# Kernel optimization log

Measured on AMD Instinct MI355X. Metric: run time of the kernel, lower is better.

The kernel has to match this reference:

```python
import jax, jax.numpy as jnp
import numpy as np

H, W, NB, BS, D = 128, 256, 8, 96, 768
HIDDEN = 4 * D
LAMBDA = 0.01  # softshrink lambda (sparsity)
EPS = 1e-5     # torch LayerNorm default eps


def layernorm(x, g, b):
    mu = jnp.mean(x, axis=-1, keepdims=True)
    var = jnp.mean((x - mu) ** 2, axis=-1, keepdims=True)
    return (x - mu) * jax.lax.rsqrt(var + EPS) * g + b


def softshrink(x, lam):
    return jnp.sign(x) * jnp.maximum(jnp.abs(x) - lam, 0.0)


def afno(x, w1, w2, b1, b2):
    # x: [B, H*W, D]; bias branch is zeros since Block constructs AFNO with bias=None
    B, HW, Dd = x.shape
    xg = x.reshape(B, H, W, Dd)
    xf = jnp.fft.rfft2(xg, axes=(1, 2), norm='ortho')          # [B, H, W//2+1, D] complex
    xf = xf.reshape(B, H, W // 2 + 1, NB, BS)
    xr, xi = jnp.real(xf), jnp.imag(xf)

    def mul(t, w):  # block-diagonal channel mixing: [..., l, m] x [l, m, n]
        return jnp.einsum('bhwlm,lmn->bhwln', t, w)

    r1 = jax.nn.relu(mul(xr, w1[0]) - mul(xi, w1[1]) + b1[0])
    i1 = jax.nn.relu(mul(xr, w1[1]) + mul(xi, w1[0]) + b1[1])
    r2 = jax.nn.relu(mul(r1, w2[0]) - mul(i1, w2[1]) + b2[0])
    i2 = jax.nn.relu(mul(r1, w2[1]) + mul(i1, w2[0]) + b2[1])
    r2 = softshrink(r2, LAMBDA)
    i2 = softshrink(i2, LAMBDA)
    xc = (r2 + 1j * i2).reshape(B, H, W // 2 + 1, Dd)
    out = jnp.fft.irfft2(xc, s=(H, W), axes=(1, 2), norm='ortho')
    return out.reshape(B, HW, Dd)


def setup_inputs() -> dict:
    key = jax.random.key(0)
    ks = jax.random.split(key, 12)
    s = 0.02
    inp = {
        'x': jax.random.normal(ks[0], (2, H * W, D), dtype=jnp.float32),
        'norm1_g': jnp.ones((D,), jnp.float32),
        'norm1_b': jnp.zeros((D,), jnp.float32),
        'w1': s * jax.random.normal(ks[1], (2, NB, BS, BS), jnp.float32),
        'w2': s * jax.random.normal(ks[2], (2, NB, BS, BS), jnp.float32),
        'b1': s * jax.random.normal(ks[3], (2, NB, BS), jnp.float32),
        'b2': s * jax.random.normal(ks[4], (2, NB, BS), jnp.float32),
        'norm2_g': jnp.ones((D,), jnp.float32),
        'norm2_b': jnp.zeros((D,), jnp.float32),
        'fc1_w': s * jax.random.normal(ks[5], (D, HIDDEN), jnp.float32),
        'fc1_b': s * jax.random.normal(ks[6], (HIDDEN,), jnp.float32),
        'fc2_w': s * jax.random.normal(ks[7], (HIDDEN, D), jnp.float32),
        'fc2_b': s * jax.random.normal(ks[8], (D,), jnp.float32),
    }
    return inp


def reference(x, norm1_g, norm1_b, w1, w2, b1, b2, norm2_g, norm2_b,
              fc1_w, fc1_b, fc2_w, fc2_b):
    residual = x
    h = layernorm(x, norm1_g, norm1_b)
    h = afno(h, w1, w2, b1, b2)          # AFNO adds zero bias internally (bias=None)
    h = layernorm(h, norm2_g, norm2_b)
    h = jax.nn.gelu(h @ fc1_w + fc1_b, approximate=False)  # torch nn.GELU default = exact erf
    h = h @ fc2_w + fc2_b
    return h + residual
```

## Files before the change

kernel.cpp:

```cpp
#include <hip/hip_runtime.h>
#include <math.h>

#define Hh 128
#define Ww 256
#define Dd 768
#define NPLANE 256
#define WF 129
#define SFREQ (WF*Dd)
#define NPOS (2*Hh*WF)
#define LAMBDA_SS 0.01f

typedef short short8 __attribute__((ext_vector_type(8)));
typedef float floatx4 __attribute__((ext_vector_type(4)));

__device__ __forceinline__ float bf2f(ushort u) {
    union { unsigned int i; float f; } v; v.i = ((unsigned int)u) << 16; return v.f;
}
__device__ __forceinline__ ushort f2bf(float f) {
    union { float f; unsigned int i; } v; v.f = f;
    unsigned int r = v.i + 0x7fffu + ((v.i >> 16) & 1u);
    return (ushort)(r >> 16);
}

__global__ __launch_bounds__(256) void ln_kernel(const float* __restrict__ x,
        const float* __restrict__ g, const float* __restrict__ b,
        ushort* __restrict__ out) {
    int row = blockIdx.x;
    int tid = threadIdx.x;
    const float* xr = x + (size_t)row * Dd;
    float v0 = xr[tid], v1 = xr[tid + 256], v2 = xr[tid + 512];
    __shared__ float red[256];
    red[tid] = v0 + v1 + v2;
    __syncthreads();
    for (int o = 128; o > 0; o >>= 1) { if (tid < o) red[tid] += red[tid + o]; __syncthreads(); }
    float mean = red[0] * (1.0f / 768.0f);
    __syncthreads();
    float d0 = v0 - mean, d1 = v1 - mean, d2 = v2 - mean;
    red[tid] = d0 * d0 + d1 * d1 + d2 * d2;
    __syncthreads();
    for (int o = 128; o > 0; o >>= 1) { if (tid < o) red[tid] += red[tid + o]; __syncthreads(); }
    float inv = rsqrtf(red[0] * (1.0f / 768.0f) + 1e-5f);
    ushort* orow = out + (size_t)row * Dd;
    orow[tid]       = f2bf(d0 * inv * g[tid]       + b[tid]);
    orow[tid + 256] = f2bf(d1 * inv * g[tid + 256] + b[tid + 256]);
    orow[tid + 512] = f2bf(d2 * inv * g[tid + 512] + b[tid + 512]);
}

#define TW_WFC_H  0
#define TW_WFC_L  65536
#define TW_WFS_H  131072
#define TW_WFS_L  196608
#define TW_HC_H   262144
#define TW_HC_L   278528
#define TW_HS_H   294912
#define TW_HS_L   311296
#define TW_HSN_H  327680
#define TW_HSN_L  344064
#define TW_WIC_H  360448
#define TW_WIC_L  401408
#define TW_WISN_H 442368
#define TW_WISN_L 483328
#define TW_TOTAL  524288

__device__ __forceinline__ void split_bf(float v, ushort* hi, ushort* lo) {
    ushort h = f2bf(v);
    *hi = h;
    *lo = f2bf(v - bf2f(h));
}

__global__ __launch_bounds__(256) void twiddle_prep_kernel(ushort* __restrict__ tw) {
    int fam = blockIdx.y;
    int idx = blockIdx.x * 256 + threadIdx.x;
    if (fam == 0) {
        if (idx >= 65536) return;
        int wf = idx >> 8, w = idx & 255;
        float c = 0.0f, s = 0.0f;
        if (wf < WF) {
            int t = (w * wf) & 255;
            float ang = (float)t * (float)(2.0 * M_PI / 256.0);
            c = cosf(ang) * 0.0625f;
            s = -sinf(ang) * 0.0625f;
        }
        split_bf(c, &tw[TW_WFC_H + idx], &tw[TW_WFC_L + idx]);
        split_bf(s, &tw[TW_WFS_H + idx], &tw[TW_WFS_L + idx]);
    } else if (fam == 1) {
        if (idx >= 16384) return;
        int a = idx >> 7, b = idx & 127;
        int t = (a * b) & 127;
        float ang = (float)t * (float)(2.0 * M_PI / 128.0);
        const float sc = 0.08838834764831845f;
        float c = cosf(ang) * sc, s = sinf(ang) * sc;
        split_bf(c,  &tw[TW_HC_H + idx],  &tw[TW_HC_L + idx]);
        split_bf(s,  &tw[TW_HS_H + idx],  &tw[TW_HS_L + idx]);
        split_bf(-s, &tw[TW_HSN_H + idx], &tw[TW_HSN_L + idx]);
    } else {
        if (idx >= 40960) return;
        int w = idx / 160, wf = idx - w * 160;
        float c = 0.0f, s = 0.0f;
        if (wf < WF) {
            int t = (w * wf) & 255;
            float ang = (float)t * (float)(2.0 * M_PI / 256.0);
            float wt = (wf == 0 || wf == 128) ? 0.5f : 1.0f;
            c = wt * cosf(ang) * 0.125f;
            s = -wt * sinf(ang) * 0.125f;
        }
        split_bf(c, &tw[TW_WIC_H + idx],  &tw[TW_WIC_L + idx]);
        split_bf(s, &tw[TW_WISN_H + idx], &tw[TW_WISN_L + idx]);
    }
}

__global__ __launch_bounds__(256) void transpose_bf_kernel(const ushort* __restrict__ in,
        ushort* __restrict__ out, int R, int C, int Rpad, size_t inB, size_t outB) {
    __shared__ ushort tile[32][33];
    int z = blockIdx.z;
    int c0 = blockIdx.x * 32, r0 = blockIdx.y * 32;
    int tx = threadIdx.x, ty = threadIdx.y;
    const ushort* ip = in + (size_t)z * inB;
    ushort* op = out + (size_t)z * outB;
    for (int j = 0; j < 32; j += 8) {
        int r = r0 + ty + j;
        tile[ty + j][tx] = (r < R) ? ip[(size_t)r * C + c0 + tx] : (ushort)0;
    }
    __syncthreads();
    for (int j = 0; j < 32; j += 8)
        op[(size_t)(c0 + ty + j) * Rpad + r0 + tx] = tile[tx][ty + j];
}

__global__ __launch_bounds__(256) void dftg_kernel(
        const ushort* __restrict__ A1h, const ushort* __restrict__ A1l,
        const ushort* __restrict__ A2h, const ushort* __restrict__ A2l,
        const ushort* __restrict__ B1, const ushort* __restrict__ B2,
        void* __restrict__ Cv, int M, int N, int K,
        size_t strideB, size_t strideC, int out_f32) {
    __shared__ __align__(16) ushort Bs1[128 * 40];
    __shared__ __align__(16) ushort Bs2[128 * 40];
    int tid = threadIdx.x;
    int bn = blockIdx.x * 128, bm = blockIdx.y * 128;
    int z = blockIdx.z;
    const ushort* b1g = B1 + (size_t)z * strideB;
    const ushort* b2g = B2 + (size_t)z * strideB;
    int wave = tid >> 6, lane = tid & 63;
    int wy = wave >> 1, wx = wave & 1;
    int quad = lane >> 4, l16 = lane & 15;
    int sr = tid >> 2, sc = (tid & 3) * 8;
    int P2 = (A2h != nullptr);

    size_t arow = (size_t)(bm + wy * 64 + l16) * K + quad * 8;
    const ushort* a1h_p = A1h + arow;
    const ushort* a1l_p = A1l + arow;
    const ushort* a2h_p = (P2 ? A2h : A1h) + arow;
    const ushort* a2l_p = (P2 ? A2l : A1l) + arow;

    floatx4 acc[4][4];
#pragma unroll
    for (int i = 0; i < 4; ++i)
#pragma unroll
        for (int j = 0; j < 4; ++j) { acc[i][j][0] = 0.f; acc[i][j][1] = 0.f; acc[i][j][2] = 0.f; acc[i][j][3] = 0.f; }

    for (int k0 = 0; k0 < K; k0 += 32) {
        uint4 b1a = *(const uint4*)(b1g + (size_t)(bn + sr) * K + k0 + sc);
        uint4 b1b = *(const uint4*)(b1g + (size_t)(bn + sr + 64) * K + k0 + sc);
        uint4 b2a, b2b;
        if (P2) {
            b2a = *(const uint4*)(b2g + (size_t)(bn + sr) * K + k0 + sc);
            b2b = *(const uint4*)(b2g + (size_t)(bn + sr + 64) * K + k0 + sc);
        }
        __syncthreads();
        *(uint4*)&Bs1[sr * 40 + sc] = b1a;
        *(uint4*)&Bs1[(sr + 64) * 40 + sc] = b1b;
        if (P2) {
            *(uint4*)&Bs2[sr * 40 + sc] = b2a;
            *(uint4*)&Bs2[(sr + 64) * 40 + sc] = b2b;
        }
        __syncthreads();
        short8 bf1[4], bf2[4];
#pragma unroll
        for (int j = 0; j < 4; ++j)
            bf1[j] = *(const short8*)&Bs1[(wx * 64 + j * 16 + l16) * 40 + quad * 8];
        if (P2) {
#pragma unroll
            for (int j = 0; j < 4; ++j)
                bf2[j] = *(const short8*)&Bs2[(wx * 64 + j * 16 + l16) * 40 + quad * 8];
        }
#pragma unroll
        for (int i = 0; i < 4; ++i) {
            size_t ao = (size_t)i * 16 * K + k0;
            short8 a1h_ = *(const short8*)(a1h_p + ao);
            short8 a1l_ = *(const short8*)(a1l_p + ao);
#pragma unroll
            for (int j = 0; j < 4; ++j) {
                acc[i][j] = __builtin_amdgcn_mfma_f32_16x16x32_bf16(a1h_, bf1[j], acc[i][j], 0, 0, 0);
                acc[i][j] = __builtin_amdgcn_mfma_f32_16x16x32_bf16(a1l_, bf1[j], acc[i][j], 0, 0, 0);
            }
            if (P2) {
                short8 a2h_ = *(const short8*)(a2h_p + ao);
                short8 a2l_ = *(const short8*)(a2l_p + ao);
#pragma unroll
                for (int j = 0; j < 4; ++j) {
                    acc[i][j] = __builtin_amdgcn_mfma_f32_16x16x32_bf16(a2h_, bf2[j], acc[i][j], 0, 0, 0);
                    acc[i][j] = __builtin_amdgcn_mfma_f32_16x16x32_bf16(a2l_, bf2[j], acc[i][j], 0, 0, 0);
                }
            }
        }
    }

#pragma unroll
    for (int i = 0; i < 4; ++i) {
        int row0 = bm + wy * 64 + i * 16 + quad * 4;
#pragma unroll
        for (int j = 0; j < 4; ++j) {
            int col = bn + wx * 64 + j * 16 + l16;
#pragma unroll
            for (int r = 0; r < 4; ++r) {
                int row = row0 + r;
                if (row < M) {
                    size_t o = (size_t)z * strideC + (size_t)row * N + col;
                    if (out_f32) ((float*)Cv)[o] = acc[i][j][r];
                    else         ((ushort*)Cv)[o] = f2bf(acc[i][j][r]);
                }
            }
        }
    }
}

__global__ __launch_bounds__(256) void wmix_prep_kernel(const float* __restrict__ w,
        ushort* __restrict__ wt) {
    int mat = blockIdx.x;
    const float* src = w + (size_t)mat * 96 * 96;
    ushort* dst = wt + (size_t)mat * 96 * 96;
    for (int idx = threadIdx.x; idx < 96 * 96; idx += 256) {
        int n = idx / 96, m = idx - n * 96;
        dst[idx] = f2bf(src[(size_t)m * 96 + n]);
    }
}

__device__ __forceinline__ short8 neg8(short8 a) {
    union { short8 s; unsigned int u[4]; } v; v.s = a;
    v.u[0] ^= 0x80008000u; v.u[1] ^= 0x80008000u;
    v.u[2] ^= 0x80008000u; v.u[3] ^= 0x80008000u;
    return v.s;
}

#define WSTR 104
__global__ __launch_bounds__(256) void mix_mfma_kernel(const ushort* __restrict__ Xr,
        const ushort* __restrict__ Xi, const ushort* __restrict__ Wt,
        const float* __restrict__ bias, ushort* __restrict__ Or,
        ushort* __restrict__ Oi, int shrink) {
    int l = blockIdx.y;
    int bm = blockIdx.x * 128;
    int tid = threadIdx.x;
    int wv = tid >> 6, lane = tid & 63;
    int quad = lane >> 4, l16 = lane & 15;

    __shared__ __align__(16) ushort Wr_s[96 * WSTR];
    __shared__ __align__(16) ushort Wi_s[96 * WSTR];
    const ushort* wr_g = Wt + (size_t)l * 96 * 96;
    const ushort* wi_g = Wt + (size_t)(8 + l) * 96 * 96;
    for (int idx = tid; idx < (96 * 96) / 4; idx += 256) {
        int n = idx / 24, mq = idx - n * 24;
        *(uint2*)&Wr_s[n * WSTR + mq * 4] = *(const uint2*)(wr_g + (size_t)n * 96 + mq * 4);
        *(uint2*)&Wi_s[n * WSTR + mq * 4] = *(const uint2*)(wi_g + (size_t)n * 96 + mq * 4);
    }

    floatx4 accr[2][6], acci[2][6];
#pragma unroll
    for (int i = 0; i < 2; ++i)
#pragma unroll
        for (int j = 0; j < 6; ++j) {
            accr[i][j][0] = 0.f; accr[i][j][1] = 0.f; accr[i][j][2] = 0.f; accr[i][j][3] = 0.f;
            acci[i][j][0] = 0.f; acci[i][j][1] = 0.f; acci[i][j][2] = 0.f; acci[i][j][3] = 0.f;
        }

    int row = bm + wv * 32 + l16;
    const ushort* agr = Xr + (size_t)row * 768 + l * 96;
    const ushort* agi = Xi + (size_t)row * 768 + l * 96;
    __syncthreads();

#pragma unroll
    for (int ks = 0; ks < 3; ++ks) {
        int ko = ks * 32 + quad * 8;
        short8 ar0 = *(const short8*)(agr + ko);
        short8 ar1 = *(const short8*)(agr + (size_t)16 * 768 + ko);
        short8 ai0 = *(const short8*)(agi + ko);
        short8 ai1 = *(const short8*)(agi + (size_t)16 * 768 + ko);
        short8 an0 = neg8(ai0), an1 = neg8(ai1);
#pragma unroll
        for (int j = 0; j < 6; ++j) {
            short8 br = *(const short8*)&Wr_s[(j * 16 + l16) * WSTR + ko];
            short8 bi = *(const short8*)&Wi_s[(j * 16 + l16) * WSTR + ko];
            accr[0][j] = __builtin_amdgcn_mfma_f32_16x16x32_bf16(ar0, br, accr[0][j], 0, 0, 0);
            accr[0][j] = __builtin_amdgcn_mfma_f32_16x16x32_bf16(an0, bi, accr[0][j], 0, 0, 0);
            acci[0][j] = __builtin_amdgcn_mfma_f32_16x16x32_bf16(ar0, bi, acci[0][j], 0, 0, 0);
            acci[0][j] = __builtin_amdgcn_mfma_f32_16x16x32_bf16(ai0, br, acci[0][j], 0, 0, 0);
            accr[1][j] = __builtin_amdgcn_mfma_f32_16x16x32_bf16(ar1, br, accr[1][j], 0, 0, 0);
            accr[1][j] = __builtin_amdgcn_mfma_f32_16x16x32_bf16(an1, bi, accr[1][j], 0, 0, 0);
            acci[1][j] = __builtin_amdgcn_mfma_f32_16x16x32_bf16(ar1, bi, acci[1][j], 0, 0, 0);
            acci[1][j] = __builtin_amdgcn_mfma_f32_16x16x32_bf16(ai1, br, acci[1][j], 0, 0, 0);
        }
    }

#pragma unroll
    for (int i = 0; i < 2; ++i) {
        int row0 = bm + wv * 32 + i * 16 + quad * 4;
#pragma unroll
        for (int j = 0; j < 6; ++j) {
            int col = j * 16 + l16;
            float bvr = bias[l * 96 + col];
            float bvi = bias[768 + l * 96 + col];
#pragma unroll
            for (int r = 0; r < 4; ++r) {
                float vr = accr[i][j][r] + bvr;
                float vi = acci[i][j][r] + bvi;
                if (shrink) { vr = fmaxf(vr - LAMBDA_SS, 0.0f); vi = fmaxf(vi - LAMBDA_SS, 0.0f); }
                else        { vr = fmaxf(vr, 0.0f);             vi = fmaxf(vi, 0.0f); }
                size_t o = (size_t)(row0 + r) * 768 + l * 96 + col;
                Or[o] = f2bf(vr);
                Oi[o] = f2bf(vi);
            }
        }
    }
}

__global__ __launch_bounds__(256) void transpose_kernel(const float* __restrict__ in,
        ushort* __restrict__ out, int R, int C) {
    __shared__ float tile[32][33];
    int c0 = blockIdx.x * 32, r0 = blockIdx.y * 32;
    int tx = threadIdx.x, ty = threadIdx.y;
    for (int j = 0; j < 32; j += 8)
        tile[ty + j][tx] = in[(size_t)(r0 + ty + j) * C + c0 + tx];
    __syncthreads();
    for (int j = 0; j < 32; j += 8)
        out[(size_t)(c0 + ty + j) * R + r0 + tx] = f2bf(tile[tx][ty + j]);
}

#define GBM 128
#define GBN 128
#define GBK 32
__global__ __launch_bounds__(256) void gemm_bt_kernel(const ushort* __restrict__ A,
        const ushort* __restrict__ Bt, void* __restrict__ Cv, int M, int N, int K,
        const float* __restrict__ bias, const float* __restrict__ resid,
        int act, int out_f32) {
    __shared__ __align__(16) ushort As[GBM * GBK];
    __shared__ __align__(16) ushort Bs[GBN * GBK];
    int tid = threadIdx.x;
    int bm = blockIdx.y * GBM, bn = blockIdx.x * GBN;
    int wave = tid >> 6, lane = tid & 63;
    int wy = wave >> 1, wx = wave & 1;
    int quad = lane >> 4, l16 = lane & 15;
    int sr = tid >> 2;
    int sc = (tid & 3) * 8;
    const ushort* Ag = A + (size_t)(bm + sr) * K + sc;
    const ushort* Bg = Bt + (size_t)(bn + sr) * K + sc;

    floatx4 acc[4][4];
#pragma unroll
    for (int i = 0; i < 4; ++i)
#pragma unroll
        for (int j = 0; j < 4; ++j) { acc[i][j][0] = 0.f; acc[i][j][1] = 0.f; acc[i][j][2] = 0.f; acc[i][j][3] = 0.f; }

    for (int k0 = 0; k0 < K; k0 += GBK) {
        uint4 a0 = *(const uint4*)(Ag + k0);
        uint4 a1 = *(const uint4*)(Ag + (size_t)64 * K + k0);
        uint4 b0 = *(const uint4*)(Bg + k0);
        uint4 b1 = *(const uint4*)(Bg + (size_t)64 * K + k0);
        __syncthreads();
        *(uint4*)&As[sr * GBK + sc] = a0;
        *(uint4*)&As[(sr + 64) * GBK + sc] = a1;
        *(uint4*)&Bs[sr * GBK + sc] = b0;
        *(uint4*)&Bs[(sr + 64) * GBK + sc] = b1;
        __syncthreads();
        short8 af[4], bfv[4];
#pragma unroll
        for (int i = 0; i < 4; ++i)
            af[i] = *(const short8*)&As[(wy * 64 + i * 16 + l16) * GBK + quad * 8];
#pragma unroll
        for (int j = 0; j < 4; ++j)
            bfv[j] = *(const short8*)&Bs[(wx * 64 + j * 16 + l16) * GBK + quad * 8];
#pragma unroll
        for (int i = 0; i < 4; ++i)
#pragma unroll
            for (int j = 0; j < 4; ++j)
                acc[i][j] = __builtin_amdgcn_mfma_f32_16x16x32_bf16(af[i], bfv[j], acc[i][j], 0, 0, 0);
    }

#pragma unroll
    for (int i = 0; i < 4; ++i) {
        int row0 = bm + wy * 64 + i * 16 + quad * 4;
#pragma unroll
        for (int j = 0; j < 4; ++j) {
            int col = bn + wx * 64 + j * 16 + l16;
            float bv = bias ? bias[col] : 0.0f;
#pragma unroll
            for (int r = 0; r < 4; ++r) {
                float v = acc[i][j][r] + bv;
                if (act == 1) v = 0.5f * v * (1.0f + erff(v * 0.70710678118f));
                size_t o = (size_t)(row0 + r) * N + col;
                if (out_f32) {
                    float vv = v + (resid ? resid[o] : 0.0f);
                    ((float*)Cv)[o] = vv;
                } else {
                    ((ushort*)Cv)[o] = f2bf(v);
                }
            }
        }
    }
}

extern "C" void kernel_launch(void* const* d_in, const int* in_sizes, int n_in,
                              void* d_out, int out_size, void* d_ws, size_t ws_size,
                              hipStream_t stream) {
    const float* x    = (const float*)d_in[0];
    const float* n1g  = (const float*)d_in[1];
    const float* n1b  = (const float*)d_in[2];
    const float* w1   = (const float*)d_in[3];
    const float* w2   = (const float*)d_in[4];
    const float* b1   = (const float*)d_in[5];
    const float* b2   = (const float*)d_in[6];
    const float* n2g  = (const float*)d_in[7];
    const float* n2b  = (const float*)d_in[8];
    const float* fc1w = (const float*)d_in[9];
    const float* fc1b = (const float*)d_in[10];
    const float* fc2w = (const float*)d_in[11];
    const float* fc2b = (const float*)d_in[12];
    float*  outf = (float*)d_out;
    ushort* outu = (ushort*)d_out;

    ushort* ws  = (ushort*)d_ws;
    ushort* W1t = ws;
    ushort* W2t = W1t + (size_t)3072 * 768;
    ushort* tw  = W2t + (size_t)768 * 3072;
    ushort* AR  = tw + TW_TOTAL;

    const size_t FSZ = (size_t)NPLANE * SFREQ;
    ushort* S1t = AR;
    ushort* FrT = AR;
    ushort* FiT = AR + FSZ;
    ushort* Mr  = AR;
    ushort* Mi  = AR + FSZ;
    ushort* NrT = AR;
    ushort* NiT = AR + FSZ;
    ushort* HrT = AR;
    ushort* HiT = AR + (size_t)256 * 768 * 160;
    ushort* Abf = AR;
    ushort* hid = AR + (size_t)65536 * 768;

    ushort* S1 = outu;
    ushort* Fr = outu;
    ushort* Fi = outu + FSZ;
    ushort* Gr = outu;
    ushort* Gi = outu + FSZ;
    ushort* Nr = outu;
    ushort* Ni = outu + FSZ;
    ushort* Hr = outu;
    ushort* Hi = outu + FSZ;
    ushort* W1mix = outu + 2 * FSZ;
    ushort* W2mix = W1mix + (size_t)2 * 8 * 96 * 96;

    transpose_kernel<<<dim3(3072 / 32, 768 / 32), dim3(32, 8), 0, stream>>>(fc1w, W1t, 768, 3072);
    transpose_kernel<<<dim3(768 / 32, 3072 / 32), dim3(32, 8), 0, stream>>>(fc2w, W2t, 3072, 768);
    wmix_prep_kernel<<<16, 256, 0, stream>>>(w1, W1mix);
    wmix_prep_kernel<<<16, 256, 0, stream>>>(w2, W2mix);
    twiddle_prep_kernel<<<dim3(256, 3), 256, 0, stream>>>(tw);

    ln_kernel<<<65536, 256, 0, stream>>>(x, n1g, n1b, S1);

    transpose_bf_kernel<<<dim3(768 / 32, 256 / 32, 256), dim3(32, 8), 0, stream>>>(
        S1, S1t, 256, 768, 256, (size_t)256 * 768, (size_t)768 * 256);
    dftg_kernel<<<dim3(768 / 128, 2, 256), 256, 0, stream>>>(
        tw + TW_WFC_H, tw + TW_WFC_L, nullptr, nullptr, S1t, S1t,
        Fr, WF, 768, 256, (size_t)768 * 256, (size_t)SFREQ, 0);
    dftg_kernel<<<dim3(768 / 128, 2, 256), 256, 0, stream>>>(
        tw + TW_WFS_H, tw + TW_WFS_L, nullptr, nullptr, S1t, S1t,
        Fi, WF, 768, 256, (size_t)768 * 256, (size_t)SFREQ, 0);

    transpose_bf_kernel<<<dim3(SFREQ / 32, 128 / 32, 2), dim3(32, 8), 0, stream>>>(
        Fr, FrT, 128, SFREQ, 128, (size_t)128 * SFREQ, (size_t)128 * SFREQ);
    transpose_bf_kernel<<<dim3(SFREQ / 32, 128 / 32, 2), dim3(32, 8), 0, stream>>>(
        Fi, FiT, 128, SFREQ, 128, (size_t)128 * SFREQ, (size_t)128 * SFREQ);
    dftg_kernel<<<dim3(SFREQ / 128, 1, 2), 256, 0, stream>>>(
        tw + TW_HC_H, tw + TW_HC_L, tw + TW_HS_H, tw + TW_HS_L, FrT, FiT,
        Gr, 128, SFREQ, 128, (size_t)128 * SFREQ, (size_t)128 * SFREQ, 0);
    dftg_kernel<<<dim3(SFREQ / 128, 1, 2), 256, 0, stream>>>(
        tw + TW_HC_H, tw + TW_HC_L, tw + TW_HSN_H, tw + TW_HSN_L, FiT, FrT,
        Gi, 128, SFREQ, 128, (size_t)128 * SFREQ, (size_t)128 * SFREQ, 0);

    mix_mfma_kernel<<<dim3(NPOS / 128, 8), 256, 0, stream>>>(Gr, Gi, W1mix, b1, Mr, Mi, 0);
    mix_mfma_kernel<<<dim3(NPOS / 128, 8), 256, 0, stream>>>(Mr, Mi, W2mix, b2, Nr, Ni, 1);

    transpose_bf_kernel<<<dim3(SFREQ / 32, 128 / 32, 2), dim3(32, 8), 0, stream>>>(
        Nr, NrT, 128, SFREQ, 128, (size_t)128 * SFREQ, (size_t)128 * SFREQ);
    transpose_bf_kernel<<<dim3(SFREQ / 32, 128 / 32, 2), dim3(32, 8), 0, stream>>>(
        Ni, NiT, 128, SFREQ, 128, (size_t)128 * SFREQ, (size_t)128 * SFREQ);
    dftg_kernel<<<dim3(SFREQ / 128, 1, 2), 256, 0, stream>>>(
        tw + TW_HC_H, tw + TW_HC_L, tw + TW_HSN_H, tw + TW_HSN_L, NrT, NiT,
        Hr, 128, SFREQ, 128, (size_t)128 * SFREQ, (size_t)128 * SFREQ, 0);
    dftg_kernel<<<dim3(SFREQ / 128, 1, 2), 256, 0, stream>>>(
        tw + TW_HC_H, tw + TW_HC_L, tw + TW_HS_H, tw + TW_HS_L, NiT, NrT,
        Hi, 128, SFREQ, 128, (size_t)128 * SFREQ, (size_t)128 * SFREQ, 0);

    transpose_bf_kernel<<<dim3(768 / 32, 5, 256), dim3(32, 8), 0, stream>>>(
        Hr, HrT, WF, 768, 160, (size_t)SFREQ, (size_t)768 * 160);
    transpose_bf_kernel<<<dim3(768 / 32, 5, 256), dim3(32, 8), 0, stream>>>(
        Hi, HiT, WF, 768, 160, (size_t)SFREQ, (size_t)768 * 160);
    dftg_kernel<<<dim3(768 / 128, 2, 256), 256, 0, stream>>>(
        tw + TW_WIC_H, tw + TW_WIC_L, tw + TW_WISN_H, tw + TW_WISN_L, HrT, HiT,
        outf, 256, 768, 160, (size_t)768 * 160, (size_t)256 * 768, 1);

    ln_kernel<<<65536, 256, 0, stream>>>(outf, n2g, n2b, Abf);

    const int CH = 8192;
    for (int c = 0; c < 8; ++c) {
        const ushort* Aln = Abf + (size_t)c * CH * 768;
        gemm_bt_kernel<<<dim3(3072 / GBN, CH / GBM), 256, 0, stream>>>(
            Aln, W1t, hid, CH, 3072, 768, fc1b, nullptr, 1, 0);
        gemm_bt_kernel<<<dim3(768 / GBN, CH / GBM), 256, 0, stream>>>(
            hid, W2t, outf + (size_t)c * CH * 768, CH, 768, 3072, fc2b,
            x + (size_t)c * CH * 768, 0, 1);
    }
}
```

Before: 3.140 ms.

## Fuse real/imag DFT GEMM pairs into single kernels with LDS-staged coalesced stores

Pairs of DFT GEMM launches that read the same B operand (real and imaginary outputs) are merged into one dftc kernel. It computes both accumulators from one staged B tile, using sign-flipped A fragments for the complex cross terms. Outputs are staged through shared memory so the kernel can write coalesced 16-byte stores instead of scattered scalar stores, and the final inverse-W DFT gets its own specialised kernel with an fp32 staged epilogue. This halves the B-operand traffic and the launch count, but doubles accumulator registers, which may cut occupancy despite the launch_bounds(256,2) hint.

Measured after the change: 2.991 ms. 4.7% less time.

```diff
diff --git a/kernel.cpp b/kernel.cpp
--- a/kernel.cpp
+++ b/kernel.cpp
@@ -20,6 +20,12 @@
     union { float f; unsigned int i; } v; v.f = f;
     unsigned int r = v.i + 0x7fffu + ((v.i >> 16) & 1u);
     return (ushort)(r >> 16);
+}
+__device__ __forceinline__ short8 neg8(short8 a) {
+    union { short8 s; unsigned int u[4]; } v; v.s = a;
+    v.u[0] ^= 0x80008000u; v.u[1] ^= 0x80008000u;
+    v.u[2] ^= 0x80008000u; v.u[3] ^= 0x80008000u;
+    return v.s;
 }
 
 __global__ __launch_bounds__(256) void ln_kernel(const float* __restrict__ x,
@@ -126,14 +132,16 @@
         op[(size_t)(c0 + ty + j) * Rpad + r0 + tx] = tile[tx][ty + j];
 }
 
-__global__ __launch_bounds__(256) void dftg_kernel(
+#define CSTR 144
+__global__ __launch_bounds__(256, 2) void dftc_kernel(
         const ushort* __restrict__ A1h, const ushort* __restrict__ A1l,
         const ushort* __restrict__ A2h, const ushort* __restrict__ A2l,
         const ushort* __restrict__ B1, const ushort* __restrict__ B2,
-        void* __restrict__ Cv, int M, int N, int K,
-        size_t strideB, size_t strideC, int out_f32) {
-    __shared__ __align__(16) ushort Bs1[128 * 40];
-    __shared__ __align__(16) ushort Bs2[128 * 40];
+        ushort* __restrict__ O1, ushort* __restrict__ O2,
+        int M, int N, int K, size_t strideB, size_t strideC, int mode) {
+    __shared__ __align__(16) ushort smem[128 * CSTR];
+    ushort* Bs1 = smem;
+    ushort* Bs2 = smem + 5120;
     int tid = threadIdx.x;
     int bn = blockIdx.x * 128, bm = blockIdx.y * 128;
     int z = blockIdx.z;
@@ -143,32 +151,34 @@
     int wy = wave >> 1, wx = wave & 1;
     int quad = lane >> 4, l16 = lane & 15;
     int sr = tid >> 2, sc = (tid & 3) * 8;
-    int P2 = (A2h != nullptr);
 
     size_t arow = (size_t)(bm + wy * 64 + l16) * K + quad * 8;
     const ushort* a1h_p = A1h + arow;
     const ushort* a1l_p = A1l + arow;
-    const ushort* a2h_p = (P2 ? A2h : A1h) + arow;
-    const ushort* a2l_p = (P2 ? A2l : A1l) + arow;
-
-    floatx4 acc[4][4];
+    const ushort* a2h_p = A2h + arow;
+    const ushort* a2l_p = A2l + arow;
+
+    floatx4 acc1[4][4], acc2[4][4];
 #pragma unroll
     for (int i = 0; i < 4; ++i)
 #pragma unroll
-        for (int j = 0; j < 4; ++j) { acc[i][j][0] = 0.f; acc[i][j][1] = 0.f; acc[i][j][2] = 0.f; acc[i][j][3] = 0.f; }
+        for (int j = 0; j < 4; ++j) {
+            acc1[i][j][0] = 0.f; acc1[i][j][1] = 0.f; acc1[i][j][2] = 0.f; acc1[i][j][3] = 0.f;
+            acc2[i][j][0] = 0.f; acc2[i][j][1] = 0.f; acc2[i][j][2] = 0.f; acc2[i][j][3] = 0.f;
+        }
 
     for (int k0 = 0; k0 < K; k0 += 32) {
         uint4 b1a = *(const uint4*)(b1g + (size_t)(bn + sr) * K + k0 + sc);
         uint4 b1b = *(const uint4*)(b1g + (size_t)(bn + sr + 64) * K + k0 + sc);
         uint4 b2a, b2b;
-        if (P2) {
+        if (mode) {
             b2a = *(const uint4*)(b2g + (size_t)(bn + sr) * K + k0 + sc);
             b2b = *(const uint4*)(b2g + (size_t)(bn + sr + 64) * K + k0 + sc);
         }
         __syncthreads();
         *(uint4*)&Bs1[sr * 40 + sc] = b1a;
         *(uint4*)&Bs1[(sr + 64) * 40 + sc] = b1b;
-        if (P2) {
+        if (mode) {
             *(uint4*)&Bs2[sr * 40 + sc] = b2a;
             *(uint4*)&Bs2[(sr + 64) * 40 + sc] = b2b;
         }
@@ -177,7 +187,7 @@
 #pragma unroll
         for (int j = 0; j < 4; ++j)
             bf1[j] = *(const short8*)&Bs1[(wx * 64 + j * 16 + l16) * 40 + quad * 8];
-        if (P2) {
+        if (mode) {
 #pragma unroll
             for (int j = 0; j < 4; ++j)
                 bf2[j] = *(const short8*)&Bs2[(wx * 64 + j * 16 + l16) * 40 + quad * 8];
@@ -187,38 +197,157 @@
             size_t ao = (size_t)i * 16 * K + k0;
             short8 a1h_ = *(const short8*)(a1h_p + ao);
             short8 a1l_ = *(const short8*)(a1l_p + ao);
+            short8 a2h_ = *(const short8*)(a2h_p + ao);
+            short8 a2l_ = *(const short8*)(a2l_p + ao);
+            if (mode) {
+#pragma unroll
+                for (int j = 0; j < 4; ++j) {
+                    acc1[i][j] = __builtin_amdgcn_mfma_f32_16x16x32_bf16(a1h_, bf1[j], acc1[i][j], 0, 0, 0);
+                    acc1[i][j] = __builtin_amdgcn_mfma_f32_16x16x32_bf16(a1l_, bf1[j], acc1[i][j], 0, 0, 0);
+                    acc1[i][j] = __builtin_amdgcn_mfma_f32_16x16x32_bf16(a2h_, bf2[j], acc1[i][j], 0, 0, 0);
+                    acc1[i][j] = __builtin_amdgcn_mfma_f32_16x16x32_bf16(a2l_, bf2[j], acc1[i][j], 0, 0, 0);
+                }
+                short8 n2h = neg8(a2h_), n2l = neg8(a2l_);
+#pragma unroll
+                for (int j = 0; j < 4; ++j) {
+                    acc2[i][j] = __builtin_amdgcn_mfma_f32_16x16x32_bf16(a1h_, bf2[j], acc2[i][j], 0, 0, 0);
+                    acc2[i][j] = __builtin_amdgcn_mfma_f32_16x16x32_bf16(a1l_, bf2[j], acc2[i][j], 0, 0, 0);
+                    acc2[i][j] = __builtin_amdgcn_mfma_f32_16x16x32_bf16(n2h, bf1[j], acc2[i][j], 0, 0, 0);
+                    acc2[i][j] = __builtin_amdgcn_mfma_f32_16x16x32_bf16(n2l, bf1[j], acc2[i][j], 0, 0, 0);
+                }
+            } else {
+#pragma unroll
+                for (int j = 0; j < 4; ++j) {
+                    acc1[i][j] = __builtin_amdgcn_mfma_f32_16x16x32_bf16(a1h_, bf1[j], acc1[i][j], 0, 0, 0);
+                    acc1[i][j] = __builtin_amdgcn_mfma_f32_16x16x32_bf16(a1l_, bf1[j], acc1[i][j], 0, 0, 0);
+                    acc2[i][j] = __builtin_amdgcn_mfma_f32_16x16x32_bf16(a2h_, bf1[j], acc2[i][j], 0, 0, 0);
+                    acc2[i][j] = __builtin_amdgcn_mfma_f32_16x16x32_bf16(a2l_, bf1[j], acc2[i][j], 0, 0, 0);
+                }
+            }
+        }
+    }
+
+    int srow = tid >> 4;
+    int schunk = (tid & 15) * 8;
+#pragma unroll
+    for (int half = 0; half < 2; ++half) {
+        ushort* Optr = half ? O2 : O1;
+        __syncthreads();
+#pragma unroll
+        for (int i = 0; i < 4; ++i) {
+            int r0 = (wy * 64 + i * 16 + quad * 4) * CSTR;
+#pragma unroll
+            for (int j = 0; j < 4; ++j) {
+                int cc = wx * 64 + j * 16 + l16;
+#pragma unroll
+                for (int r = 0; r < 4; ++r) {
+                    float v = half ? acc2[i][j][r] : acc1[i][j][r];
+                    smem[r0 + r * CSTR + cc] = f2bf(v);
+                }
+            }
+        }
+        __syncthreads();
+#pragma unroll
+        for (int p = 0; p < 8; ++p) {
+            int row = p * 16 + srow;
+            int grow = bm + row;
+            if (grow < M) {
+                uint4 v = *(const uint4*)&smem[row * CSTR + schunk];
+                *(uint4*)&Optr[(size_t)z * strideC + (size_t)grow * N + bn + schunk] = v;
+            }
+        }
+    }
+}
+
+__global__ __launch_bounds__(256, 2) void dftwi_kernel(
+        const ushort* __restrict__ A1h, const ushort* __restrict__ A1l,
+        const ushort* __restrict__ A2h, const ushort* __restrict__ A2l,
+        const ushort* __restrict__ B1, const ushort* __restrict__ B2,
+        float* __restrict__ O, int M, int N, int K, size_t strideB, size_t strideC) {
+    __shared__ __align__(16) ushort smem[128 * CSTR];
+    ushort* Bs1 = smem;
+    ushort* Bs2 = smem + 5120;
+    float* Csf = (float*)smem;
+    int tid = threadIdx.x;
+    int bn = blockIdx.x * 128, bm = blockIdx.y * 128;
+    int z = blockIdx.z;
+    const ushort* b1g = B1 + (size_t)z * strideB;
+    const ushort* b2g = B2 + (size_t)z * strideB;
+    int wave = tid >> 6, lane = tid & 63;
+    int wy = wave >> 1, wx = wave & 1;
+    int quad = lane >> 4, l16 = lane & 15;
+    int sr = tid >> 2, sc = (tid & 3) * 8;
+
+    size_t arow = (size_t)(bm + wy * 64 + l16) * K + quad * 8;
+    const ushort* a1h_p = A1h + arow;
+    const ushort* a1l_p = A1l + arow;
+    const ushort* a2h_p = A2h + arow;
+    const ushort* a2l_p = A2l + arow;
+
+    floatx4 acc[4][4];
+#pragma unroll
+    for (int i = 0; i < 4; ++i)
+#pragma unroll
+        for (int j = 0; j < 4; ++j) { acc[i][j][0] = 0.f; acc[i][j][1] = 0.f; acc[i][j][2] = 0.f; acc[i][j][3] = 0.f; }
+
+    for (int k0 = 0; k0 < K; k0 += 32) {
+        uint4 b1a = *(const uint4*)(b1g + (size_t)(bn + sr) * K + k0 + sc);
+        uint4 b1b = *(const uint4*)(b1g + (size_t)(bn + sr + 64) * K + k0 + sc);
+        uint4 b2a = *(const uint4*)(b2g + (size_t)(bn + sr) * K + k0 + sc);
+        uint4 b2b = *(const uint4*)(b2g + (size_t)(bn + sr + 64) * K + k0 + sc);
+        __syncthreads();
+        *(uint4*)&Bs1[sr * 40 + sc] = b1a;
+        *(uint4*)&Bs1[(sr + 64) * 40 + sc] = b1b;
+        *(uint4*)&Bs2[sr * 40 + sc] = b2a;
+        *(uint4*)&Bs2[(sr + 64) * 40 + sc] = b2b;
+        __syncthreads();
+        short8 bf1[4], bf2[4];
+#pragma unroll
+        for (int j = 0; j < 4; ++j) {
+            bf1[j] = *(const short8*)&Bs1[(wx * 64 + j * 16 + l16) * 40 + quad * 8];
+            bf2[j] = *(const short8*)&Bs2[(wx * 64 + j * 16 + l16) * 40 + quad * 8];
+        }
+#pragma unroll
+        for (int i = 0; i < 4; ++i) {
+            size_t ao = (size_t)i * 16 * K + k0;
+            short8 a1h_ = *(const short8*)(a1h_p + ao);
+            short8 a1l_ = *(const short8*)(a1l_p + ao);
+            short8 a2h_ = *(const short8*)(a2h_p + ao);
+            short8 a2l_ = *(const short8*)(a2l_p + ao);
 #pragma unroll
             for (int j = 0; j < 4; ++j) {
                 acc[i][j] = __builtin_amdgcn_mfma_f32_16x16x32_bf16(a1h_, bf1[j], acc[i][j], 0, 0, 0);
                 acc[i][j] = __builtin_amdgcn_mfma_f32_16x16x32_bf16(a1l_, bf1[j], acc[i][j], 0, 0, 0);
+                acc[i][j] = __builtin_amdgcn_mfma_f32_16x16x32_bf16(a2h_, bf2[j], acc[i][j], 0, 0, 0);
+                acc[i][j] = __builtin_amdgcn_mfma_f32_16x16x32_bf16(a2l_, bf2[j], acc[i][j], 0, 0, 0);
             }
-            if (P2) {
-                short8 a2h_ = *(const short8*)(a2h_p + ao);
-                short8 a2l_ = *(const short8*)(a2l_p + ao);
+        }
+    }
+
+    int srow = tid >> 5;
+    int chunk = (tid & 31) * 4;
+#pragma unroll
+    for (int h = 0; h < 2; ++h) {
+        __syncthreads();
+        if (wy == h) {
+#pragma unroll
+            for (int i = 0; i < 4; ++i) {
+                int r0 = (i * 16 + quad * 4) * CSTR;
 #pragma unroll
                 for (int j = 0; j < 4; ++j) {
-                    acc[i][j] = __builtin_amdgcn_mfma_f32_16x16x32_bf16(a2h_, bf2[j], acc[i][j], 0, 0, 0);
-                    acc[i][j] = __builtin_amdgcn_mfma_f32_16x16x32_bf16(a2l_, bf2[j], acc[i][j], 0, 0, 0);
+                    int cc = wx * 64 + j * 16 + l16;
+#pragma unroll
+                    for (int r = 0; r < 4; ++r)
+                        Csf[r0 + r * CSTR + cc] = acc[i][j][r];
                 }
             }
         }
-    }
-
-#pragma unroll
-    for (int i = 0; i < 4; ++i) {
-        int row0 = bm + wy * 64 + i * 16 + quad * 4;
-#pragma unroll
-        for (int j = 0; j < 4; ++j) {
-            int col = bn + wx * 64 + j * 16 + l16;
-#pragma unroll
-            for (int r = 0; r < 4; ++r) {
-                int row = row0 + r;
-                if (row < M) {
-                    size_t o = (size_t)z * strideC + (size_t)row * N + col;
-                    if (out_f32) ((float*)Cv)[o] = acc[i][j][r];
-                    else         ((ushort*)Cv)[o] = f2bf(acc[i][j][r]);
-                }
-            }
+        __syncthreads();
+#pragma unroll
+        for (int p = 0; p < 8; ++p) {
+            int row = p * 8 + srow;
+            uint4 v = *(const uint4*)&Csf[row * CSTR + chunk];
+            *(uint4*)&O[(size_t)z * strideC + (size_t)(bm + h * 64 + row) * N + bn + chunk] = v;
         }
     }
 }
@@ -232,13 +361,6 @@
         int n = idx / 96, m = idx - n * 96;
         dst[idx] = f2bf(src[(size_t)m * 96 + n]);
     }
-}
-
-__device__ __forceinline__ short8 neg8(short8 a) {
-    union { short8 s; unsigned int u[4]; } v; v.s = a;
-    v.u[0] ^= 0x80008000u; v.u[1] ^= 0x80008000u;
-    v.u[2] ^= 0x80008000u; v.u[3] ^= 0x80008000u;
-    return v.s;
 }
 
 #define WSTR 104
@@ -466,23 +588,17 @@
 
     transpose_bf_kernel<<<dim3(768 / 32, 256 / 32, 256), dim3(32, 8), 0, stream>>>(
         S1, S1t, 256, 768, 256, (size_t)256 * 768, (size_t)768 * 256);
-    dftg_kernel<<<dim3(768 / 128, 2, 256), 256, 0, stream>>>(
-        tw + TW_WFC_H, tw + TW_WFC_L, nullptr, nullptr, S1t, S1t,
-        Fr, WF, 768, 256, (size_t)768 * 256, (size_t)SFREQ, 0);
-    dftg_kernel<<<dim3(768 / 128, 2, 256), 256, 0, stream>>>(
-        tw + TW_WFS_H, tw + TW_WFS_L, nullptr, nullptr, S1t, S1t,
-        Fi, WF, 768, 256, (size_t)768 * 256, (size_t)SFREQ, 0);
+    dftc_kernel<<<dim3(768 / 128, 2, 256), 256, 0, stream>>>(
+        tw + TW_WFC_H, tw + TW_WFC_L, tw + TW_WFS_H, tw + TW_WFS_L,
+        S1t, S1t, Fr, Fi, WF, 768, 256, (size_t)768 * 256, (size_t)SFREQ, 0);
 
     transpose_bf_kernel<<<dim3(SFREQ / 32, 128 / 32, 2), dim3(32, 8), 0, stream>>>(
         Fr, FrT, 128, SFREQ, 128, (size_t)128 * SFREQ, (size_t)128 * SFREQ);
     transpose_bf_kernel<<<dim3(SFREQ / 32, 128 / 32, 2), dim3(32, 8), 0, stream>>>(
         Fi, FiT, 128, SFREQ, 128, (size_t)128 * SFREQ, (size_t)128 * SFREQ);
-    dftg_kernel<<<dim3(SFREQ / 128, 1, 2), 256, 0, stream>>>(
-        tw + TW_HC_H, tw + TW_HC_L, tw + TW_HS_H, tw + TW_HS_L, FrT, FiT,
-        Gr, 128, SFREQ, 128, (size_t)128 * SFREQ, (size_t)128 * SFREQ, 0);
-    dftg_kernel<<<dim3(SFREQ / 128, 1, 2), 256, 0, stream>>>(
-        tw + TW_HC_H, tw + TW_HC_L, tw + TW_HSN_H, tw + TW_HSN_L, FiT, FrT,
-        Gi, 128, SFREQ, 128, (size_t)128 * SFREQ, (size_t)128 * SFREQ, 0);
+    dftc_kernel<<<dim3(SFREQ / 128, 1, 2), 256, 0, stream>>>(
+        tw + TW_HC_H, tw + TW_HC_L, tw + TW_HS_H, tw + TW_HS_L,
+        FrT, FiT, Gr, Gi, 128, SFREQ, 128, (size_t)128 * SFREQ, (size_t)128 * SFREQ, 1);
 
     mix_mfma_kernel<<<dim3(NPOS / 128, 8), 256, 0, stream>>>(Gr, Gi, W1mix, b1, Mr, Mi, 0);
     mix_mfma_kernel<<<dim3(NPOS / 128, 8), 256, 0, stream>>>(Mr, Mi, W2mix, b2, Nr, Ni, 1);
@@ -491,20 +607,17 @@
         Nr, NrT, 128, SFREQ, 128, (size_t)128 * SFREQ, (size_t)128 * SFREQ);
     transpose_bf_kernel<<<dim3(SFREQ / 32, 128 / 32, 2), dim3(32, 8), 0, stream>>>(
         Ni, NiT, 128, SFREQ, 128, (size_t)128 * SFREQ, (size_t)128 * SFREQ);
-    dftg_kernel<<<dim3(SFREQ / 128, 1, 2), 256, 0, stream>>>(
-        tw + TW_HC_H, tw + TW_HC_L, tw + TW_HSN_H, tw + TW_HSN_L, NrT, NiT,
-        Hr, 128, SFREQ, 128, (size_t)128 * SFREQ, (size_t)128 * SFREQ, 0);
-    dftg_kernel<<<dim3(SFREQ / 128, 1, 2), 256, 0, stream>>>(
-        tw + TW_HC_H, tw + TW_HC_L, tw + TW_HS_H, tw + TW_HS_L, NiT, NrT,
-        Hi, 128, SFREQ, 128, (size_t)128 * SFREQ, (size_t)128 * SFREQ, 0);
+    dftc_kernel<<<dim3(SFREQ / 128, 1, 2), 256, 0, stream>>>(
+        tw + TW_HC_H, tw + TW_HC_L, tw + TW_HS_H, tw + TW_HS_L,
+        NiT, NrT, Hi, Hr, 128, SFREQ, 128, (size_t)128 * SFREQ, (size_t)128 * SFREQ, 1);
 
     transpose_bf_kernel<<<dim3(768 / 32, 5, 256), dim3(32, 8), 0, stream>>>(
         Hr, HrT, WF, 768, 160, (size_t)SFREQ, (size_t)768 * 160);
     transpose_bf_kernel<<<dim3(768 / 32, 5, 256), dim3(32, 8), 0, stream>>>(
         Hi, HiT, WF, 768, 160, (size_t)SFREQ, (size_t)768 * 160);
-    dftg_kernel<<<dim3(768 / 128, 2, 256), 256, 0, stream>>>(
-        tw + TW_WIC_H, tw + TW_WIC_L, tw + TW_WISN_H, tw + TW_WISN_L, HrT, HiT,
-        outf, 256, 768, 160, (size_t)768 * 160, (size_t)256 * 768, 1);
+    dftwi_kernel<<<dim3(768 / 128, 2, 256), 256, 0, stream>>>(
+        tw + TW_WIC_H, tw + TW_WIC_L, tw + TW_WISN_H, tw + TW_WISN_L,
+        HrT, HiT, outf, 256, 768, 160, (size_t)768 * 160, (size_t)256 * 768);
 
     ln_kernel<<<65536, 256, 0, stream>>>(outf, n2g, n2b, Abf);
 
```
